# Optimization experiments

Measured on AMD Instinct MI355X. Metric: run time of the kernel, lower is better.

## Reference

```python
import jax, jax.numpy as jnp
import numpy as np

EPS = 1e-5
SLOPE = 0.2


def _ico_conv(x, neigh, w, b):
    # x: (B, C, N); neigh: (N, 7) -> gather 1-ring, flatten channel-major, linear
    g = x[:, :, neigh]                          # (B, C, N, 7)
    B, C, N, K = g.shape
    g = g.transpose(0, 2, 1, 3).reshape(B, N, C * K)
    y = jnp.einsum('bnf,of->bno', g, w) + b     # (B, N, out)
    return y.transpose(0, 2, 1)                 # (B, out, N)


def _bn(x, gamma, beta):
    # BatchNorm1d with track_running_stats=False: batch stats over (B, N)
    mean = x.mean(axis=(0, 2), keepdims=True)
    var = x.var(axis=(0, 2), keepdims=True)
    xhat = (x - mean) * jax.lax.rsqrt(var + EPS)
    return xhat * gamma[None, :, None] + beta[None, :, None]


def _lrelu(x):
    return jnp.where(x >= 0, x, SLOPE * x)


def setup_inputs() -> dict:
    key = jax.random.key(0)
    ks = jax.random.split(key, 10)
    B, IN_CH, OUT_CH = 2, 128, 64
    N_DOWN, N_UP, K = 40962, 163842, 7
    inp = {
        'x1': jax.random.normal(ks[0], (B, IN_CH, N_DOWN), jnp.float32),
        'x2': jax.random.normal(ks[1], (B, OUT_CH, N_UP), jnp.float32),
        'up_fc_w': jax.random.normal(ks[2], (OUT_CH, IN_CH), jnp.float32) * 0.05,
        'up_fc_b': jax.random.normal(ks[3], (OUT_CH,), jnp.float32) * 0.05,
        'conv1_w': jax.random.normal(ks[4], (OUT_CH, K * IN_CH), jnp.float32) * 0.05,
        'conv1_b': jax.random.normal(ks[5], (OUT_CH,), jnp.float32) * 0.05,
        'bn1_g': jnp.ones((OUT_CH,), jnp.float32),
        'bn1_b': jnp.zeros((OUT_CH,), jnp.float32),
        'conv2_w': jax.random.normal(ks[6], (OUT_CH, K * OUT_CH), jnp.float32) * 0.05,
        'conv2_b': jax.random.normal(ks[7], (OUT_CH,), jnp.float32) * 0.05,
        'bn2_g': jnp.ones((OUT_CH,), jnp.float32),
        'bn2_b': jnp.zeros((OUT_CH,), jnp.float32),
        'up_neigh': jax.random.randint(ks[8], (N_UP, 2), 0, N_DOWN, jnp.int32),
        'conv_neigh': jax.random.randint(ks[9], (N_UP, K), 0, N_UP, jnp.int32),
        'max_pool_indices': jnp.zeros((1,), jnp.int32),  # unused for up_mode='interp'
    }
    return inp


def reference(x1, x2, up_fc_w, up_fc_b, conv1_w, conv1_b, bn1_g, bn1_b,
              conv2_w, conv2_b, bn2_g, bn2_b, up_neigh, conv_neigh,
              max_pool_indices):
    # --- IcoUpSampleLayer ('interp'): Linear(in->out) then 2-neighbor mean ---
    h = jnp.einsum('bcn,oc->bno', x1, up_fc_w) + up_fc_b   # (B, N_down, out)
    h = h[:, up_neigh].mean(axis=2)                        # (B, N_up, out)
    x1_up = h.transpose(0, 2, 1)                           # (B, out, N_up)
    # --- concat skip along channels ---
    x = jnp.concatenate([x1_up, x2], axis=1)               # (B, in_ch, N_up)
    # --- (conv => BN => LeakyReLU) * 2 ---
    x = _lrelu(_bn(_ico_conv(x, conv_neigh, conv1_w, conv1_b), bn1_g, bn1_b))
    x = _lrelu(_bn(_ico_conv(x, conv_neigh, conv2_w, conv2_b), bn2_g, bn2_b))
    return x
```

## Files before the change

### kernel.cpp

```cpp
#include <hip/hip_runtime.h>
#include <hip/hip_bf16.h>

typedef __hip_bfloat16 bf16;
typedef short bf16x8 __attribute__((ext_vector_type(8)));
typedef float f32x4 __attribute__((ext_vector_type(4)));

#define ND     40962
#define NUP    163842
#define NBATCH 2
#define NTC    2561
#define BN_EPS 1e-5
#define SLOPE  0.2f

#define OFF_W1P   0ull
#define OFF_W2P   114688ull
#define OFF_STATS 172032ull
#define OFF_H     173056ull
#define OFF_P2    (OFF_H + 2622464ull)
#define OFF_HM    10659328ull
#define OFF_X2T   52602880ull
#define OFF_Y     94546432ull

__device__ __forceinline__ void gload_lds16(const void* g, void* l) {
  __builtin_amdgcn_global_load_lds(
      (const __attribute__((address_space(1))) void*)g,
      (__attribute__((address_space(3))) void*)l, 16, 0, 0);
}

__device__ __forceinline__ float lrelu(float v) { return v >= 0.0f ? v : SLOPE * v; }

__global__ __launch_bounds__(256) void k_permw(const float* __restrict__ w1,
                                               const float* __restrict__ w2,
                                               bf16* __restrict__ w1p, bf16* __restrict__ w2p) {
  int t = blockIdx.x * 256 + threadIdx.x;
  if (t < 64 * 896) {
    int o = t / 896, f = t % 896;
    int kk = f / 128, c = f % 128;
    w1p[t] = __float2bfloat16(w1[o * 896 + c * 7 + kk]);
  } else if (t < 64 * 896 + 64 * 448) {
    int idx = t - 64 * 896;
    int o = idx / 448, f = idx % 448;
    int kk = f / 64, c = f % 64;
    w2p[idx] = __float2bfloat16(w2[o * 448 + c * 7 + kk]);
  }
}

__global__ __launch_bounds__(256) void k_h(const float* __restrict__ x1,
                                           const float* __restrict__ wfc,
                                           const float* __restrict__ bfc,
                                           bf16* __restrict__ h) {
  __shared__ float wl[128 * 64];
  __shared__ float bl[64];
  int tid = threadIdx.x, b = blockIdx.y;
  for (int i = tid; i < 8192; i += 256) { int o = i >> 7, c = i & 127; wl[c * 64 + o] = wfc[i]; }
  if (tid < 64) bl[tid] = bfc[tid];
  __syncthreads();
  int n = blockIdx.x * 256 + tid;
  int nc = n < ND ? n : ND - 1;
  float acc[64];
#pragma unroll
  for (int o = 0; o < 64; ++o) acc[o] = bl[o];
#pragma unroll 4
  for (int c = 0; c < 128; ++c) {
    float xv = x1[((size_t)b * 128 + c) * (size_t)ND + nc];
    const f32x4* wrow = (const f32x4*)(wl + c * 64);
#pragma unroll
    for (int og = 0; og < 16; ++og) {
      f32x4 wv = wrow[og];
      acc[og * 4 + 0] = fmaf(xv, wv[0], acc[og * 4 + 0]);
      acc[og * 4 + 1] = fmaf(xv, wv[1], acc[og * 4 + 1]);
      acc[og * 4 + 2] = fmaf(xv, wv[2], acc[og * 4 + 2]);
      acc[og * 4 + 3] = fmaf(xv, wv[3], acc[og * 4 + 3]);
    }
  }
  if (n < ND) {
    bf16* hp = h + ((size_t)b * ND + n) * 64;
#pragma unroll
    for (int og = 0; og < 8; ++og) {
      union { bf16x8 v; bf16 e[8]; } u;
#pragma unroll
      for (int j = 0; j < 8; ++j) u.e[j] = __float2bfloat16(acc[og * 8 + j]);
      ((bf16x8*)hp)[og] = u.v;
    }
  }
}

__global__ __launch_bounds__(256) void k_hm(const bf16* __restrict__ h,
                                            const int* __restrict__ upn,
                                            bf16* __restrict__ hm) {
  __shared__ int un[64][2];
  int tid = threadIdx.x, b = blockIdx.y;
  int m0 = blockIdx.x * 64;
  if (tid < 128) {
    int ml = tid >> 1, w = tid & 1;
    int m = m0 + ml; if (m >= NUP) m = NUP - 1;
    un[ml][w] = upn[(size_t)m * 2 + w];
  }
  __syncthreads();
  int ln = tid >> 2, sg = tid & 3;
  int m = m0 + ln;
  if (m >= NUP) return;
  const bf16* h0 = h + ((size_t)b * ND + un[ln][0]) * 64 + sg * 16;
  const bf16* h1 = h + ((size_t)b * ND + un[ln][1]) * 64 + sg * 16;
  bf16* d = hm + ((size_t)b * NUP + m) * 64 + sg * 16;
#pragma unroll
  for (int q = 0; q < 2; ++q) {
    union { bf16x8 v; bf16 e[8]; } a, bb, o_;
    a.v = ((const bf16x8*)h0)[q];
    bb.v = ((const bf16x8*)h1)[q];
#pragma unroll
    for (int j = 0; j < 8; ++j)
      o_.e[j] = __float2bfloat16(0.5f * (__bfloat162float(a.e[j]) + __bfloat162float(bb.e[j])));
    ((bf16x8*)d)[q] = o_.v;
  }
}

__global__ __launch_bounds__(256) void k_x2t(const float* __restrict__ x2,
                                             bf16* __restrict__ x2t) {
  __shared__ float tt[64][65];
  int tid = threadIdx.x, b = blockIdx.y;
  int m0 = blockIdx.x * 64;
#pragma unroll
  for (int i = 0; i < 16; ++i) {
    int c = i * 4 + (tid >> 6);
    int ml = tid & 63;
    int m = m0 + ml; if (m >= NUP) m = NUP - 1;
    tt[c][ml] = x2[((size_t)b * 64 + c) * (size_t)NUP + m];
  }
  __syncthreads();
  int ln = tid >> 2, sg = tid & 3;
  int m = m0 + ln;
  if (m >= NUP) return;
  bf16* d = x2t + ((size_t)b * NUP + m) * 64 + sg * 16;
#pragma unroll
  for (int q = 0; q < 2; ++q) {
    union { bf16x8 v; bf16 e[8]; } o_;
#pragma unroll
    for (int j = 0; j < 8; ++j) o_.e[j] = __float2bfloat16(tt[sg * 16 + q * 8 + j][ln]);
    ((bf16x8*)d)[q] = o_.v;
  }
}

__global__ __launch_bounds__(256, 8) void k_conv1(const bf16* __restrict__ hm,
                                                  const bf16* __restrict__ x2t,
                                                  const int* __restrict__ neigh,
                                                  const bf16* __restrict__ wp,
                                                  const float* __restrict__ bias,
                                                  bf16* __restrict__ y,
                                                  float* __restrict__ partials) {
  constexpr int NSTEP = 28;
  __shared__ bf16 lA[2][2048];
  __shared__ bf16 lW[2][2048];
  __shared__ int nbl[448];

  int tid = threadIdx.x, b = blockIdx.y;
  int n0 = blockIdx.x * 64;
  int wv = tid >> 6, lane = tid & 63;
  int l15 = lane & 15, l4 = lane >> 4;

  for (int j = tid; j < 448; j += 256) {
    int gi = n0 * 7 + j;
    int gmax = NUP * 7 - 1;
    nbl[j] = neigh[gi <= gmax ? gi : gmax];
  }

  f32x4 acc[4];
#pragma unroll
  for (int ot = 0; ot < 4; ++ot) {
    float bv = bias[ot * 16 + l15];
    acc[ot] = (f32x4){bv, bv, bv, bv};
  }

  const bf16* hmb  = hm  + (size_t)b * NUP * 64;
  const bf16* x2tb = x2t + (size_t)b * NUP * 64;
  const int srow = wv * 16 + (lane >> 2);
  const int sg   = ((lane & 3) ^ ((srow >> 1) & 3)) * 8;
  const bf16* wrow_ = wp + (size_t)srow * 896 + sg;

  auto STAGE = [&](int buf, int t) {
    int kk = t >> 2, ks = t & 3;
    int node = nbl[srow * 7 + kk];
    const bf16* src = (ks < 2) ? (hmb + (size_t)node * 64 + ks * 32)
                               : (x2tb + (size_t)node * 64 + (ks - 2) * 32);
    gload_lds16(src + sg, &lA[buf][wv * 512]);
    gload_lds16(wrow_ + kk * 128 + ks * 32, &lW[buf][wv * 512]);
  };

  const int r  = wv * 16 + l15;
  const int oa = r * 32 + ((l4 ^ ((l15 >> 1) & 3)) * 8);

  __syncthreads();
  STAGE(0, 0);
  __syncthreads();

  int buf = 0;
#pragma unroll
  for (int t = 0; t < NSTEP; ++t) {
    if (t + 1 < NSTEP) STAGE(buf ^ 1, t + 1);
    bf16x8 a = *(const bf16x8*)(&lA[buf][oa]);
#pragma unroll
    for (int ot = 0; ot < 4; ++ot) {
      int o = ot * 16 + l15;
      bf16x8 bb = *(const bf16x8*)(&lW[buf][o * 32 + ((l4 ^ ((l15 >> 1) & 3)) * 8)]);
      acc[ot] = __builtin_amdgcn_mfma_f32_16x16x32_bf16(a, bb, acc[ot], 0, 0, 0);
    }
    __syncthreads();
    buf ^= 1;
  }

  float* lred = (float*)&lA[0][0];
  float s[4], q[4];
#pragma unroll
  for (int ot = 0; ot < 4; ++ot) { s[ot] = 0.0f; q[ot] = 0.0f; }
  bf16* yb = y + (size_t)b * NUP * 64;
  int nodebase = n0 + wv * 16 + l4 * 4;
#pragma unroll
  for (int i = 0; i < 4; ++i) {
    int node = nodebase + i;
    bool ok = node < NUP;
#pragma unroll
    for (int ot = 0; ot < 4; ++ot) {
      float v = acc[ot][i];
      if (ok) {
        yb[(size_t)node * 64 + ot * 16 + l15] = __float2bfloat16(v);
        s[ot] += v; q[ot] += v * v;
      }
    }
  }
#pragma unroll
  for (int ot = 0; ot < 4; ++ot) {
    s[ot] += __shfl_xor(s[ot], 16); s[ot] += __shfl_xor(s[ot], 32);
    q[ot] += __shfl_xor(q[ot], 16); q[ot] += __shfl_xor(q[ot], 32);
  }
  if (lane < 16) {
#pragma unroll
    for (int ot = 0; ot < 4; ++ot) {
      lred[(wv * 2 + 0) * 64 + ot * 16 + lane] = s[ot];
      lred[(wv * 2 + 1) * 64 + ot * 16 + lane] = q[ot];
    }
  }
  __syncthreads();
  if (tid < 128) {
    int which = tid >> 6, c = tid & 63;
    float p = lred[(0 * 2 + which) * 64 + c] + lred[(1 * 2 + which) * 64 + c] +
              lred[(2 * 2 + which) * 64 + c] + lred[(3 * 2 + which) * 64 + c];
    partials[((size_t)b * gridDim.x + blockIdx.x) * 128 + which * 64 + c] = p;
  }
}

__global__ __launch_bounds__(256, 8) void k_conv2(const bf16* __restrict__ y,
                                                  const int* __restrict__ neigh,
                                                  const bf16* __restrict__ wp,
                                                  const float* __restrict__ bias,
                                                  const float* __restrict__ sc,
                                                  const float* __restrict__ sh,
                                                  bf16* __restrict__ y2,
                                                  float* __restrict__ partials) {
  constexpr int NSTEP = 14;
  __shared__ bf16 lA[2][2048];
  __shared__ bf16 lW[2][2048];
  __shared__ int nbl[448];
  __shared__ float ssc[64], ssh[64];

  int tid = threadIdx.x, b = blockIdx.y;
  int n0 = blockIdx.x * 64;
  int wv = tid >> 6, lane = tid & 63;
  int l15 = lane & 15, l4 = lane >> 4;

  for (int j = tid; j < 448; j += 256) {
    int gi = n0 * 7 + j;
    int gmax = NUP * 7 - 1;
    nbl[j] = neigh[gi <= gmax ? gi : gmax];
  }
  if (tid < 64) { ssc[tid] = sc[tid]; ssh[tid] = sh[tid]; }

  f32x4 acc[4];
#pragma unroll
  for (int ot = 0; ot < 4; ++ot) {
    float bv = bias[ot * 16 + l15];
    acc[ot] = (f32x4){bv, bv, bv, bv};
  }

  const bf16* yb = y + (size_t)b * NUP * 64;
  const int srow = wv * 16 + (lane >> 2);
  const int seg  = lane & 3;
  const int slot = (seg ^ ((srow >> 1) & 3)) * 8;
  const bf16* wrow_ = wp + (size_t)srow * 448 + slot;

  bf16x8 anext;
  auto STAGE_W = [&](int buf, int t) {
    int kk = t >> 1, ks = t & 1;
    gload_lds16(wrow_ + kk * 64 + ks * 32, &lW[buf][wv * 512]);
  };
  auto ALOAD = [&](int t) {
    int kk = t >> 1, ks = t & 1;
    int node = nbl[srow * 7 + kk];
    anext = *(const bf16x8*)(yb + (size_t)node * 64 + ks * 32 + seg * 8);
  };
  auto BNW = [&](int buf, int t) {
    int ks = t & 1;
    union { bf16x8 v; bf16 e[8]; } u, o_;
    u.v = anext;
#pragma unroll
    for (int j = 0; j < 8; ++j) {
      int c = ks * 32 + seg * 8 + j;
      float f = __bfloat162float(u.e[j]);
      o_.e[j] = __float2bfloat16(lrelu(fmaf(f, ssc[c], ssh[c])));
    }
    *(bf16x8*)(&lA[buf][srow * 32 + slot]) = o_.v;
  };

  const int r  = wv * 16 + l15;
  const int oa = r * 32 + ((l4 ^ ((l15 >> 1) & 3)) * 8);

  __syncthreads();
  STAGE_W(0, 0); ALOAD(0);
  __syncthreads();
  BNW(0, 0);

  int buf = 0;
#pragma unroll
  for (int t = 0; t < NSTEP; ++t) {
    if (t + 1 < NSTEP) { STAGE_W(buf ^ 1, t + 1); ALOAD(t + 1); }
    bf16x8 a = *(const bf16x8*)(&lA[buf][oa]);
#pragma unroll
    for (int ot = 0; ot < 4; ++ot) {
      int o = ot * 16 + l15;
      bf16x8 bb = *(const bf16x8*)(&lW[buf][o * 32 + ((l4 ^ ((l15 >> 1) & 3)) * 8)]);
      acc[ot] = __builtin_amdgcn_mfma_f32_16x16x32_bf16(a, bb, acc[ot], 0, 0, 0);
    }
    __syncthreads();
    if (t + 1 < NSTEP) BNW(buf ^ 1, t + 1);
    buf ^= 1;
  }

  float* lred = (float*)&lA[0][0];
  float s[4], q[4];
#pragma unroll
  for (int ot = 0; ot < 4; ++ot) { s[ot] = 0.0f; q[ot] = 0.0f; }
  bf16* yo = y2 + (size_t)b * NUP * 64;
  int nodebase = n0 + wv * 16 + l4 * 4;
#pragma unroll
  for (int i = 0; i < 4; ++i) {
    int node = nodebase + i;
    bool ok = node < NUP;
#pragma unroll
    for (int ot = 0; ot < 4; ++ot) {
      float v = acc[ot][i];
      if (ok) {
        yo[(size_t)node * 64 + ot * 16 + l15] = __float2bfloat16(v);
        s[ot] += v; q[ot] += v * v;
      }
    }
  }
#pragma unroll
  for (int ot = 0; ot < 4; ++ot) {
    s[ot] += __shfl_xor(s[ot], 16); s[ot] += __shfl_xor(s[ot], 32);
    q[ot] += __shfl_xor(q[ot], 16); q[ot] += __shfl_xor(q[ot], 32);
  }
  if (lane < 16) {
#pragma unroll
    for (int ot = 0; ot < 4; ++ot) {
      lred[(wv * 2 + 0) * 64 + ot * 16 + lane] = s[ot];
      lred[(wv * 2 + 1) * 64 + ot * 16 + lane] = q[ot];
    }
  }
  __syncthreads();
  if (tid < 128) {
    int which = tid >> 6, c = tid & 63;
    float p = lred[(0 * 2 + which) * 64 + c] + lred[(1 * 2 + which) * 64 + c] +
              lred[(2 * 2 + which) * 64 + c] + lred[(3 * 2 + which) * 64 + c];
    partials[((size_t)b * gridDim.x + blockIdx.x) * 128 + which * 64 + c] = p;
  }
}

__global__ __launch_bounds__(256) void k_red1(const float* __restrict__ p, int nblk,
                                              float* __restrict__ p2) {
  int g = blockIdx.x * 2 + threadIdx.x / 128;
  int j = threadIdx.x & 127;
  float a = 0.0f;
  for (int r = g; r < nblk; r += 128) a += p[(size_t)r * 128 + j];
  p2[(size_t)g * 128 + j] = a;
}

__global__ __launch_bounds__(128) void k_stats(const float* __restrict__ p2,
                                               const float* __restrict__ g,
                                               const float* __restrict__ be,
                                               float* __restrict__ sc, float* __restrict__ sh) {
  __shared__ double red[128];
  int j = threadIdx.x;
  double a = 0.0;
  for (int r = 0; r < 128; ++r) a += (double)p2[r * 128 + j];
  red[j] = a;
  __syncthreads();
  if (j < 64) {
    double M = (double)NBATCH * (double)NUP;
    double mean = red[j] / M;
    double var = red[64 + j] / M - mean * mean;
    float s = g[j] * (float)(1.0 / sqrt(var + BN_EPS));
    sc[j] = s;
    sh[j] = be[j] - (float)mean * s;
  }
}

__global__ __launch_bounds__(256) void k_final(const bf16* __restrict__ y,
                                               const float* __restrict__ sc,
                                               const float* __restrict__ sh,
                                               float* __restrict__ out) {
  __shared__ float t[64][65];
  __shared__ float ssc[64], ssh[64];
  int tid = threadIdx.x, b = blockIdx.y;
  int n0 = blockIdx.x * 64;
  if (tid < 64) { ssc[tid] = sc[tid]; ssh[tid] = sh[tid]; }
  __syncthreads();
  int ln = tid >> 2, qc = tid & 3;
  int n = n0 + ln; if (n >= NUP) n = NUP - 1;
  const bf16* yp = y + ((size_t)b * NUP + n) * 64 + qc * 16;
  union { bf16x8 v; bf16 el[8]; } v0, v1;
  v0.v = ((const bf16x8*)yp)[0];
  v1.v = ((const bf16x8*)yp)[1];
#pragma unroll
  for (int j = 0; j < 8; ++j) {
    int c = qc * 16 + j;
    t[ln][c] = lrelu(fmaf(__bfloat162float(v0.el[j]), ssc[c], ssh[c]));
  }
#pragma unroll
  for (int j = 0; j < 8; ++j) {
    int c = qc * 16 + 8 + j;
    t[ln][c] = lrelu(fmaf(__bfloat162float(v1.el[j]), ssc[c], ssh[c]));
  }
  __syncthreads();
  int nl = tid & 63;
  int nn = n0 + nl;
  if (nn >= NUP) return;
#pragma unroll
  for (int i = 0; i < 16; ++i) {
    int c = i * 4 + (tid >> 6);
    out[((size_t)b * 64 + c) * (size_t)NUP + nn] = t[nl][c];
  }
}

extern "C" void kernel_launch(void* const* d_in, const int* in_sizes, int n_in,
                              void* d_out, int out_size, void* d_ws, size_t ws_size,
                              hipStream_t stream) {
  const float* x1      = (const float*)d_in[0];
  const float* x2      = (const float*)d_in[1];
  const float* up_fc_w = (const float*)d_in[2];
  const float* up_fc_b = (const float*)d_in[3];
  const float* conv1_w = (const float*)d_in[4];
  const float* conv1_b = (const float*)d_in[5];
  const float* bn1_g   = (const float*)d_in[6];
  const float* bn1_b   = (const float*)d_in[7];
  const float* conv2_w = (const float*)d_in[8];
  const float* conv2_b = (const float*)d_in[9];
  const float* bn2_g   = (const float*)d_in[10];
  const float* bn2_b   = (const float*)d_in[11];
  const int* up_neigh  = (const int*)d_in[12];
  const int* conv_nei  = (const int*)d_in[13];

  char* ws = (char*)d_ws;
  bf16*  w1p  = (bf16*)(ws + OFF_W1P);
  bf16*  w2p  = (bf16*)(ws + OFF_W2P);
  float* sc   = (float*)(ws + OFF_STATS);
  float* sh   = sc + 64;
  bf16*  h    = (bf16*)(ws + OFF_H);
  float* part = (float*)(ws + OFF_H);
  float* p2   = (float*)(ws + OFF_P2);
  bf16*  hm   = (bf16*)(ws + OFF_HM);
  bf16*  y2   = (bf16*)(ws + OFF_HM);
  bf16*  x2t  = (bf16*)(ws + OFF_X2T);
  bf16*  y    = (bf16*)(ws + OFF_Y);
  float* out  = (float*)d_out;

  k_permw<<<336, 256, 0, stream>>>(conv1_w, conv2_w, w1p, w2p);
  k_h<<<dim3(161, 2), 256, 0, stream>>>(x1, up_fc_w, up_fc_b, h);
  k_hm<<<dim3(NTC, 2), 256, 0, stream>>>(h, up_neigh, hm);
  k_x2t<<<dim3(NTC, 2), 256, 0, stream>>>(x2, x2t);
  k_conv1<<<dim3(NTC, 2), 256, 0, stream>>>(hm, x2t, conv_nei, w1p, conv1_b, y, part);
  k_red1<<<64, 256, 0, stream>>>(part, 2 * NTC, p2);
  k_stats<<<1, 128, 0, stream>>>(p2, bn1_g, bn1_b, sc, sh);
  k_conv2<<<dim3(NTC, 2), 256, 0, stream>>>(y, conv_nei, w2p, conv2_b, sc, sh, y2, part);
  k_red1<<<64, 256, 0, stream>>>(part, 2 * NTC, p2);
  k_stats<<<1, 128, 0, stream>>>(p2, bn2_g, bn2_b, sc, sh);
  k_final<<<dim3(NTC, 2), 256, 0, stream>>>(y2, sc, sh, out);
}
```

Before: 336.5 us.

## Widen conv K-steps to 64, fuse prep kernels, split k_h outputs across waves

Each conv pipeline step now covers a full 64-channel neighbor row instead of 32 channels. This halves the number of barrier-separated steps and issues two MFMAs per A fragment, with a new XOR swizzle for the 64-wide LDS rows. conv2 drops to a single padded A buffer and gets an extra barrier before the reduction. The x2 transpose and upsample-mean kernels are merged into one launch, and k_h now spreads the 64 outputs across 4 waves so it launches more blocks with fewer registers each. The larger LDS tiles lower the occupancy bounds (8 to 4 and 6 blocks), and the single A buffer in conv2 serializes the BN write against the MFMA reads.

```diff
diff --git a/kernel.cpp b/kernel.cpp
--- a/kernel.cpp
+++ b/kernel.cpp
@@ -55,28 +55,29 @@
   for (int i = tid; i < 8192; i += 256) { int o = i >> 7, c = i & 127; wl[c * 64 + o] = wfc[i]; }
   if (tid < 64) bl[tid] = bfc[tid];
   __syncthreads();
-  int n = blockIdx.x * 256 + tid;
+  int ln = tid & 63, wv = tid >> 6;
+  int n = blockIdx.x * 64 + ln;
   int nc = n < ND ? n : ND - 1;
-  float acc[64];
-#pragma unroll
-  for (int o = 0; o < 64; ++o) acc[o] = bl[o];
+  float acc[16];
+#pragma unroll
+  for (int j = 0; j < 16; ++j) acc[j] = bl[wv * 16 + j];
 #pragma unroll 4
   for (int c = 0; c < 128; ++c) {
     float xv = x1[((size_t)b * 128 + c) * (size_t)ND + nc];
-    const f32x4* wrow = (const f32x4*)(wl + c * 64);
-#pragma unroll
-    for (int og = 0; og < 16; ++og) {
-      f32x4 wv = wrow[og];
-      acc[og * 4 + 0] = fmaf(xv, wv[0], acc[og * 4 + 0]);
-      acc[og * 4 + 1] = fmaf(xv, wv[1], acc[og * 4 + 1]);
-      acc[og * 4 + 2] = fmaf(xv, wv[2], acc[og * 4 + 2]);
-      acc[og * 4 + 3] = fmaf(xv, wv[3], acc[og * 4 + 3]);
+    const f32x4* wrow = (const f32x4*)(wl + c * 64 + wv * 16);
+#pragma unroll
+    for (int g = 0; g < 4; ++g) {
+      f32x4 wvv = wrow[g];
+      acc[g * 4 + 0] = fmaf(xv, wvv[0], acc[g * 4 + 0]);
+      acc[g * 4 + 1] = fmaf(xv, wvv[1], acc[g * 4 + 1]);
+      acc[g * 4 + 2] = fmaf(xv, wvv[2], acc[g * 4 + 2]);
+      acc[g * 4 + 3] = fmaf(xv, wvv[3], acc[g * 4 + 3]);
     }
   }
   if (n < ND) {
-    bf16* hp = h + ((size_t)b * ND + n) * 64;
-#pragma unroll
-    for (int og = 0; og < 8; ++og) {
+    bf16* hp = h + ((size_t)b * ND + n) * 64 + wv * 16;
+#pragma unroll
+    for (int og = 0; og < 2; ++og) {
       union { bf16x8 v; bf16 e[8]; } u;
 #pragma unroll
       for (int j = 0; j < 8; ++j) u.e[j] = __float2bfloat16(acc[og * 8 + j]);
@@ -85,39 +86,13 @@
   }
 }
 
-__global__ __launch_bounds__(256) void k_hm(const bf16* __restrict__ h,
-                                            const int* __restrict__ upn,
-                                            bf16* __restrict__ hm) {
+__global__ __launch_bounds__(256) void k_prep(const float* __restrict__ x2,
+                                              const bf16* __restrict__ h,
+                                              const int* __restrict__ upn,
+                                              bf16* __restrict__ hm,
+                                              bf16* __restrict__ x2t) {
+  __shared__ float tt[64][65];
   __shared__ int un[64][2];
-  int tid = threadIdx.x, b = blockIdx.y;
-  int m0 = blockIdx.x * 64;
-  if (tid < 128) {
-    int ml = tid >> 1, w = tid & 1;
-    int m = m0 + ml; if (m >= NUP) m = NUP - 1;
-    un[ml][w] = upn[(size_t)m * 2 + w];
-  }
-  __syncthreads();
-  int ln = tid >> 2, sg = tid & 3;
-  int m = m0 + ln;
-  if (m >= NUP) return;
-  const bf16* h0 = h + ((size_t)b * ND + un[ln][0]) * 64 + sg * 16;
-  const bf16* h1 = h + ((size_t)b * ND + un[ln][1]) * 64 + sg * 16;
-  bf16* d = hm + ((size_t)b * NUP + m) * 64 + sg * 16;
-#pragma unroll
-  for (int q = 0; q < 2; ++q) {
-    union { bf16x8 v; bf16 e[8]; } a, bb, o_;
-    a.v = ((const bf16x8*)h0)[q];
-    bb.v = ((const bf16x8*)h1)[q];
-#pragma unroll
-    for (int j = 0; j < 8; ++j)
-      o_.e[j] = __float2bfloat16(0.5f * (__bfloat162float(a.e[j]) + __bfloat162float(bb.e[j])));
-    ((bf16x8*)d)[q] = o_.v;
-  }
-}
-
-__global__ __launch_bounds__(256) void k_x2t(const float* __restrict__ x2,
-                                             bf16* __restrict__ x2t) {
-  __shared__ float tt[64][65];
   int tid = threadIdx.x, b = blockIdx.y;
   int m0 = blockIdx.x * 64;
 #pragma unroll
@@ -127,30 +102,52 @@
     int m = m0 + ml; if (m >= NUP) m = NUP - 1;
     tt[c][ml] = x2[((size_t)b * 64 + c) * (size_t)NUP + m];
   }
-  __syncthreads();
-  int ln = tid >> 2, sg = tid & 3;
+  if (tid < 128) {
+    int ml = tid >> 1, w = tid & 1;
+    int m = m0 + ml; if (m >= NUP) m = NUP - 1;
+    un[ml][w] = upn[(size_t)m * 2 + w];
+  }
+  __syncthreads();
+  int ln = tid >> 2, p = tid & 3;
   int m = m0 + ln;
   if (m >= NUP) return;
-  bf16* d = x2t + ((size_t)b * NUP + m) * 64 + sg * 16;
-#pragma unroll
-  for (int q = 0; q < 2; ++q) {
-    union { bf16x8 v; bf16 e[8]; } o_;
-#pragma unroll
-    for (int j = 0; j < 8; ++j) o_.e[j] = __float2bfloat16(tt[sg * 16 + q * 8 + j][ln]);
-    ((bf16x8*)d)[q] = o_.v;
-  }
-}
-
-__global__ __launch_bounds__(256, 8) void k_conv1(const bf16* __restrict__ hm,
+  {
+    const bf16* h0 = h + ((size_t)b * ND + un[ln][0]) * 64 + p * 16;
+    const bf16* h1 = h + ((size_t)b * ND + un[ln][1]) * 64 + p * 16;
+    bf16* d = hm + ((size_t)b * NUP + m) * 64 + p * 16;
+#pragma unroll
+    for (int q = 0; q < 2; ++q) {
+      union { bf16x8 v; bf16 e[8]; } a, bb, o_;
+      a.v = ((const bf16x8*)h0)[q];
+      bb.v = ((const bf16x8*)h1)[q];
+#pragma unroll
+      for (int j = 0; j < 8; ++j)
+        o_.e[j] = __float2bfloat16(0.5f * (__bfloat162float(a.e[j]) + __bfloat162float(bb.e[j])));
+      ((bf16x8*)d)[q] = o_.v;
+    }
+  }
+  {
+    bf16* d = x2t + ((size_t)b * NUP + m) * 64 + p * 16;
+#pragma unroll
+    for (int q = 0; q < 2; ++q) {
+      union { bf16x8 v; bf16 e[8]; } o_;
+#pragma unroll
+      for (int j = 0; j < 8; ++j) o_.e[j] = __float2bfloat16(tt[p * 16 + q * 8 + j][ln]);
+      ((bf16x8*)d)[q] = o_.v;
+    }
+  }
+}
+
+__global__ __launch_bounds__(256, 4) void k_conv1(const bf16* __restrict__ hm,
                                                   const bf16* __restrict__ x2t,
                                                   const int* __restrict__ neigh,
                                                   const bf16* __restrict__ wp,
                                                   const float* __restrict__ bias,
                                                   bf16* __restrict__ y,
                                                   float* __restrict__ partials) {
-  constexpr int NSTEP = 28;
-  __shared__ bf16 lA[2][2048];
-  __shared__ bf16 lW[2][2048];
+  constexpr int NSTEP = 14;
+  __shared__ bf16 lA[2][64 * 64];
+  __shared__ bf16 lW[2][64 * 64];
   __shared__ int nbl[448];
 
   int tid = threadIdx.x, b = blockIdx.y;
@@ -173,21 +170,22 @@
 
   const bf16* hmb  = hm  + (size_t)b * NUP * 64;
   const bf16* x2tb = x2t + (size_t)b * NUP * 64;
-  const int srow = wv * 16 + (lane >> 2);
-  const int sg   = ((lane & 3) ^ ((srow >> 1) & 3)) * 8;
-  const bf16* wrow_ = wp + (size_t)srow * 896 + sg;
+  const int lrow = lane >> 3;
+  const int g    = ((lane & 7) ^ lrow) * 8;
 
   auto STAGE = [&](int buf, int t) {
-    int kk = t >> 2, ks = t & 3;
-    int node = nbl[srow * 7 + kk];
-    const bf16* src = (ks < 2) ? (hmb + (size_t)node * 64 + ks * 32)
-                               : (x2tb + (size_t)node * 64 + (ks - 2) * 32);
-    gload_lds16(src + sg, &lA[buf][wv * 512]);
-    gload_lds16(wrow_ + kk * 128 + ks * 32, &lW[buf][wv * 512]);
+    int kk = t >> 1;
+    const bf16* src = (t & 1) ? x2tb : hmb;
+#pragma unroll
+    for (int i = 0; i < 2; ++i) {
+      int srow = wv * 16 + i * 8 + lrow;
+      int node = nbl[srow * 7 + kk];
+      gload_lds16(src + (size_t)node * 64 + g, &lA[buf][(wv * 16 + i * 8) * 64]);
+      gload_lds16(wp + (size_t)srow * 896 + t * 64 + g, &lW[buf][(wv * 16 + i * 8) * 64]);
+    }
   };
 
-  const int r  = wv * 16 + l15;
-  const int oa = r * 32 + ((l4 ^ ((l15 >> 1) & 3)) * 8);
+  const int r = wv * 16 + l15;
 
   __syncthreads();
   STAGE(0, 0);
@@ -197,12 +195,16 @@
 #pragma unroll
   for (int t = 0; t < NSTEP; ++t) {
     if (t + 1 < NSTEP) STAGE(buf ^ 1, t + 1);
-    bf16x8 a = *(const bf16x8*)(&lA[buf][oa]);
-#pragma unroll
-    for (int ot = 0; ot < 4; ++ot) {
-      int o = ot * 16 + l15;
-      bf16x8 bb = *(const bf16x8*)(&lW[buf][o * 32 + ((l4 ^ ((l15 >> 1) & 3)) * 8)]);
-      acc[ot] = __builtin_amdgcn_mfma_f32_16x16x32_bf16(a, bb, acc[ot], 0, 0, 0);
+#pragma unroll
+    for (int ks = 0; ks < 2; ++ks) {
+      int sa = ks * 4 + l4;
+      bf16x8 a = *(const bf16x8*)(&lA[buf][r * 64 + ((sa ^ (r & 7)) * 8)]);
+#pragma unroll
+      for (int ot = 0; ot < 4; ++ot) {
+        int o = ot * 16 + l15;
+        bf16x8 bb = *(const bf16x8*)(&lW[buf][o * 64 + ((sa ^ (o & 7)) * 8)]);
+        acc[ot] = __builtin_amdgcn_mfma_f32_16x16x32_bf16(a, bb, acc[ot], 0, 0, 0);
+      }
     }
     __syncthreads();
     buf ^= 1;
@@ -248,7 +250,7 @@
   }
 }
 
-__global__ __launch_bounds__(256, 8) void k_conv2(const bf16* __restrict__ y,
+__global__ __launch_bounds__(256, 6) void k_conv2(const bf16* __restrict__ y,
                                                   const int* __restrict__ neigh,
                                                   const bf16* __restrict__ wp,
                                                   const float* __restrict__ bias,
@@ -256,9 +258,9 @@
                                                   const float* __restrict__ sh,
                                                   bf16* __restrict__ y2,
                                                   float* __restrict__ partials) {
-  constexpr int NSTEP = 14;
-  __shared__ bf16 lA[2][2048];
-  __shared__ bf16 lW[2][2048];
+  constexpr int NSTEP = 7;
+  __shared__ bf16 lA[64 * 66];
+  __shared__ bf16 lW[2][64 * 64];
   __shared__ int nbl[448];
   __shared__ float ssc[64], ssh[64];
 
@@ -282,59 +284,70 @@
   }
 
   const bf16* yb = y + (size_t)b * NUP * 64;
-  const int srow = wv * 16 + (lane >> 2);
-  const int seg  = lane & 3;
-  const int slot = (seg ^ ((srow >> 1) & 3)) * 8;
-  const bf16* wrow_ = wp + (size_t)srow * 448 + slot;
-
-  bf16x8 anext;
-  auto STAGE_W = [&](int buf, int t) {
-    int kk = t >> 1, ks = t & 1;
-    gload_lds16(wrow_ + kk * 64 + ks * 32, &lW[buf][wv * 512]);
+  const int lrow = lane >> 3;
+  const int slot = lane & 7;
+  const int gw   = (slot ^ lrow) * 8;
+
+  bf16x8 anext[2];
+  auto STAGE_W = [&](int buf, int kk) {
+#pragma unroll
+    for (int i = 0; i < 2; ++i) {
+      int srow = wv * 16 + i * 8 + lrow;
+      gload_lds16(wp + (size_t)srow * 448 + kk * 64 + gw, &lW[buf][(wv * 16 + i * 8) * 64]);
+    }
   };
-  auto ALOAD = [&](int t) {
-    int kk = t >> 1, ks = t & 1;
-    int node = nbl[srow * 7 + kk];
-    anext = *(const bf16x8*)(yb + (size_t)node * 64 + ks * 32 + seg * 8);
+  auto ALOAD = [&](int kk) {
+#pragma unroll
+    for (int i = 0; i < 2; ++i) {
+      int srow = wv * 16 + i * 8 + lrow;
+      int node = nbl[srow * 7 + kk];
+      anext[i] = *(const bf16x8*)(yb + (size_t)node * 64 + slot * 8);
+    }
   };
-  auto BNW = [&](int buf, int t) {
-    int ks = t & 1;
-    union { bf16x8 v; bf16 e[8]; } u, o_;
-    u.v = anext;
-#pragma unroll
-    for (int j = 0; j < 8; ++j) {
-      int c = ks * 32 + seg * 8 + j;
-      float f = __bfloat162float(u.e[j]);
-      o_.e[j] = __float2bfloat16(lrelu(fmaf(f, ssc[c], ssh[c])));
-    }
-    *(bf16x8*)(&lA[buf][srow * 32 + slot]) = o_.v;
+  auto BNW = [&]() {
+#pragma unroll
+    for (int i = 0; i < 2; ++i) {
+      int srow = wv * 16 + i * 8 + lrow;
+      union { bf16x8 v; bf16 e[8]; } u, o_;
+      u.v = anext[i];
+#pragma unroll
+      for (int j = 0; j < 8; ++j) {
+        int c = slot * 8 + j;
+        float f = __bfloat162float(u.e[j]);
+        o_.e[j] = __float2bfloat16(lrelu(fmaf(f, ssc[c], ssh[c])));
+      }
+      *(bf16x8*)(&lA[srow * 66 + slot * 8]) = o_.v;
+    }
   };
 
-  const int r  = wv * 16 + l15;
-  const int oa = r * 32 + ((l4 ^ ((l15 >> 1) & 3)) * 8);
+  const int r = wv * 16 + l15;
 
   __syncthreads();
   STAGE_W(0, 0); ALOAD(0);
   __syncthreads();
-  BNW(0, 0);
+  BNW();
 
   int buf = 0;
 #pragma unroll
   for (int t = 0; t < NSTEP; ++t) {
     if (t + 1 < NSTEP) { STAGE_W(buf ^ 1, t + 1); ALOAD(t + 1); }
-    bf16x8 a = *(const bf16x8*)(&lA[buf][oa]);
-#pragma unroll
-    for (int ot = 0; ot < 4; ++ot) {
-      int o = ot * 16 + l15;
-      bf16x8 bb = *(const bf16x8*)(&lW[buf][o * 32 + ((l4 ^ ((l15 >> 1) & 3)) * 8)]);
-      acc[ot] = __builtin_amdgcn_mfma_f32_16x16x32_bf16(a, bb, acc[ot], 0, 0, 0);
+#pragma unroll
+    for (int ks = 0; ks < 2; ++ks) {
+      int sa = ks * 4 + l4;
+      bf16x8 a = *(const bf16x8*)(&lA[r * 66 + sa * 8]);
+#pragma unroll
+      for (int ot = 0; ot < 4; ++ot) {
+        int o = ot * 16 + l15;
+        bf16x8 bb = *(const bf16x8*)(&lW[buf][o * 64 + ((sa ^ (o & 7)) * 8)]);
+        acc[ot] = __builtin_amdgcn_mfma_f32_16x16x32_bf16(a, bb, acc[ot], 0, 0, 0);
+      }
     }
     __syncthreads();
-    if (t + 1 < NSTEP) BNW(buf ^ 1, t + 1);
+    if (t + 1 < NSTEP) BNW();
     buf ^= 1;
   }
 
-  float* lred = (float*)&lA[0][0];
+  float* lred = (float*)&lA[0];
   float s[4], q[4];
 #pragma unroll
   for (int ot = 0; ot < 4; ++ot) { s[ot] = 0.0f; q[ot] = 0.0f; }
@@ -358,6 +371,7 @@
     s[ot] += __shfl_xor(s[ot], 16); s[ot] += __shfl_xor(s[ot], 32);
     q[ot] += __shfl_xor(q[ot], 16); q[ot] += __shfl_xor(q[ot], 32);
   }
+  __syncthreads();
   if (lane < 16) {
 #pragma unroll
     for (int ot = 0; ot < 4; ++ot) {
@@ -473,9 +487,8 @@
   float* out  = (float*)d_out;
 
   k_permw<<<336, 256, 0, stream>>>(conv1_w, conv2_w, w1p, w2p);
-  k_h<<<dim3(161, 2), 256, 0, stream>>>(x1, up_fc_w, up_fc_b, h);
-  k_hm<<<dim3(NTC, 2), 256, 0, stream>>>(h, up_neigh, hm);
-  k_x2t<<<dim3(NTC, 2), 256, 0, stream>>>(x2, x2t);
+  k_h<<<dim3(641, 2), 256, 0, stream>>>(x1, up_fc_w, up_fc_b, h);
+  k_prep<<<dim3(NTC, 2), 256, 0, stream>>>(x2, h, up_neigh, hm, x2t);
   k_conv1<<<dim3(NTC, 2), 256, 0, stream>>>(hm, x2t, conv_nei, w1p, conv1_b, y, part);
   k_red1<<<64, 256, 0, stream>>>(part, 2 * NTC, p2);
   k_stats<<<1, 128, 0, stream>>>(p2, bn1_g, bn1_b, sc, sh);
```

After: 332.5 us (median of 2 runs). About the same (-1.2%).
